# Performance work log

Measured on AMD Instinct MI355X. Metric: run time of the kernel, lower is better.

The kernel has to match this reference:

```python
import jax, jax.numpy as jnp
import numpy as np


def log_g(x):
    # log of g(x) = where(x>=0, x+0.5, sigmoid(x))
    return jnp.where(x >= 0, jnp.log(jax.nn.relu(x) + 0.5), -jax.nn.softplus(-x))


def heinsen_associative_scan_log(log_coeffs, log_values):
    a_star = jnp.cumsum(log_coeffs, axis=1)
    log_h0_plus_b_star = jax.lax.cumlogsumexp(log_values - a_star, axis=1)
    return jnp.exp(a_star + log_h0_plus_b_star)


def setup_inputs() -> dict:
    key = jax.random.key(0)
    k1, k2 = jax.random.split(key)
    B, T, D = 4, 8192, 512
    x = jax.random.normal(k1, (B, T, D), dtype=jnp.float32)
    # Linear(dim, 2*dim, bias=False); scaled like torch default init
    W = jax.random.normal(k2, (D, 2 * D), dtype=jnp.float32) * (1.0 / np.sqrt(D))
    return {"x": x, "W": W}


def reference(x, W):
    hg = jnp.einsum('btd,de->bte', x, W)  # [B,T,2D]
    hidden, gate = jnp.split(hg, 2, axis=-1)
    log_z = -jax.nn.softplus(-gate)       # log sigmoid(gate)
    log_coeffs = -jax.nn.softplus(gate)   # log (1 - sigmoid(gate))
    log_tilde_h = log_g(hidden)
    out = heinsen_associative_scan_log(log_coeffs, log_z + log_tilde_h)
    return out
```

## Files before the change

### kernel.cpp

```cpp
#include <hip/hip_runtime.h>

typedef unsigned short u16;
typedef unsigned int   u32;

typedef __bf16 bf16x8 __attribute__((ext_vector_type(8)));
typedef float  f32x4  __attribute__((ext_vector_type(4)));

#define B_DIM 4
#define T_DIM 8192
#define D_DIM 512
#define M_DIM (B_DIM * T_DIM)
#define K_DIM D_DIM
#define NC    256
#define LCH   32

__device__ __forceinline__ u16 f2bf(float f) {
  u32 u = __float_as_uint(f);
  u32 r = (u + 0x7FFFu + ((u >> 16) & 1u)) >> 16;
  return (u16)r;
}
__device__ __forceinline__ float bf2f(u16 b) {
  return __uint_as_float(((u32)b) << 16);
}

__device__ __forceinline__ void gload_lds16(const u16* g, u16* lds) {
  __builtin_amdgcn_global_load_lds(
      (const __attribute__((address_space(1))) void*)g,
      (__attribute__((address_space(3))) void*)lds, 16, 0, 0);
}


__global__ void convert_x(const float4* __restrict__ in, u16* __restrict__ out, int n4) {
  int i = blockIdx.x * blockDim.x + threadIdx.x;
  int stride = gridDim.x * blockDim.x;
  for (; i < n4; i += stride) {
    float4 f = in[i];
    u32 w0 = (u32)f2bf(f.x) | ((u32)f2bf(f.y) << 16);
    u32 w1 = (u32)f2bf(f.z) | ((u32)f2bf(f.w) << 16);
    *reinterpret_cast<uint2*>(out + (size_t)i * 4) = make_uint2(w0, w1);
  }
}

__global__ void convert_wt(const float* __restrict__ W, u16* __restrict__ wt) {
  int idx = blockIdx.x * blockDim.x + threadIdx.x;
  int n  = idx & 1023;
  int k0 = (idx >> 10) * 8;
  float f[8];
#pragma unroll
  for (int j = 0; j < 8; ++j) f[j] = W[(size_t)(k0 + j) * 1024 + n];
  u32 w[4];
#pragma unroll
  for (int j = 0; j < 4; ++j)
    w[j] = (u32)f2bf(f[2 * j]) | ((u32)f2bf(f[2 * j + 1]) << 16);
  *reinterpret_cast<uint4*>(wt + (size_t)n * 512 + k0) = make_uint4(w[0], w[1], w[2], w[3]);
}


#define BK 32
#define NT 16

__global__ __launch_bounds__(512, 4) void gemm_act(const u16* __restrict__ xb,
                                                   const u16* __restrict__ wt,
                                                   u32* __restrict__ av_buf,
                                                   float* __restrict__ Asum,
                                                   float* __restrict__ Bsum) {
  __shared__ u16 As[3][8192];
  __shared__ u16 Bs[3][4096];

  const int tid  = threadIdx.x;
  const int lane = tid & 63;
  const int wave = tid >> 6;
  const int l15  = lane & 15;
  const int lh   = lane >> 4;
  const int wr   = wave >> 1;
  const int wc   = wave & 1;
  const int m_base = blockIdx.x * 256;
  const int d0     = blockIdx.y * 64;

  const int pairl = tid >> 3;
  const int slog  = (tid & 7) ^ (pairl & 7);
  const int lrow  = (pairl << 1) | (slog >> 2);
  const int scol  = (slog & 3) << 3;
  const int garow0 = m_base + lrow;
  const int garow1 = garow0 + 128;
  const int pB = lrow >> 5;
  const int gn = ((pB & 1) ? 512 : 0) + d0 + ((pB >> 1) << 5) + (lrow & 31);
  const int ldsw = wave * 512;

  f32x4 acc[4][4];
#pragma unroll
  for (int m = 0; m < 4; ++m)
#pragma unroll
    for (int n = 0; n < 4; ++n)
      acc[m][n] = (f32x4){0.f, 0.f, 0.f, 0.f};

#define STAGE(buf, kt)                                                      \
  do {                                                                      \
    const int ko = (kt) * BK + scol;                                        \
    gload_lds16(xb + (size_t)garow0 * K_DIM + ko, &As[buf][ldsw]);          \
    gload_lds16(xb + (size_t)garow1 * K_DIM + ko, &As[buf][4096 + ldsw]);   \
    gload_lds16(wt + (size_t)gn * K_DIM + ko, &Bs[buf][ldsw]);              \
  } while (0)

#define AOFF(row) (((row) >> 1) * 64 + (((((((row) & 1) << 2) | lh)) ^ (((row) >> 1) & 7)) << 3))

#define COMPUTE(cur)                                                        \
  do {                                                                      \
    bf16x8 af[4], bfr[4];                                                   \
    _Pragma("unroll")                                                       \
    for (int m = 0; m < 4; ++m)                                             \
      af[m] = *reinterpret_cast<const bf16x8*>(&As[cur][AOFF(64 * wr + 16 * m + l15)]); \
    _Pragma("unroll")                                                       \
    for (int n = 0; n < 4; ++n)                                             \
      bfr[n] = *reinterpret_cast<const bf16x8*>(&Bs[cur][AOFF(64 * wc + 16 * n + l15)]); \
    _Pragma("unroll")                                                       \
    for (int m = 0; m < 4; ++m)                                             \
      _Pragma("unroll")                                                     \
      for (int n = 0; n < 4; ++n)                                           \
        acc[m][n] = __builtin_amdgcn_mfma_f32_16x16x32_bf16(af[m], bfr[n], acc[m][n], 0, 0, 0); \
  } while (0)

#define WAITV(N) asm volatile("s_waitcnt vmcnt(" #N ")" ::: "memory")
#define BAR()    asm volatile("s_barrier" ::: "memory")

  STAGE(0, 0);
  STAGE(1, 1);
#pragma unroll
  for (int t = 0; t < 14; ++t) {
    WAITV(3);
    BAR();
    STAGE((t + 2) % 3, t + 2);
    COMPUTE(t % 3);
  }
  WAITV(3); BAR(); COMPUTE(2);
  WAITV(0); BAR(); COMPUTE(0);
#undef STAGE
#undef COMPUTE
#undef WAITV
#undef BAR

  const int row_w = m_base + 64 * wr;
#pragma unroll
  for (int h = 0; h < 2; ++h) {
    float Ar[2][2], Br[2][2];
#pragma unroll
    for (int mm = 0; mm < 2; ++mm) {
      const int m = 2 * h + mm;
#pragma unroll
      for (int n = 0; n < 2; ++n) {
        float A = 1.f, Bv = 0.f;
        const int dch = d0 + 32 * wc + 16 * n + l15;
#pragma unroll
        for (int r = 0; r < 4; ++r) {
          float hid = acc[m][n][r];
          float gt  = acc[m][n + 2][r];
          float e   = __expf(gt);
          float inv = 1.f / (1.f + e);
          float g   = (hid >= 0.f) ? (hid + 0.5f) : (1.f / (1.f + __expf(-hid)));
          float v   = (e * inv) * g;
          u16 abf = f2bf(inv);
          u16 vbf = f2bf(v);
          const int grow = row_w + 16 * m + 4 * lh + r;
          av_buf[(size_t)grow * D_DIM + dch] = (u32)abf | ((u32)vbf << 16);
          float af = bf2f(abf), vf = bf2f(vbf);
          Bv = af * Bv + vf;
          A *= af;
        }
        Ar[n][mm] = A; Br[n][mm] = Bv;
      }
    }
#pragma unroll
    for (int n = 0; n < 2; ++n)
#pragma unroll
      for (int mm = 0; mm < 2; ++mm) {
        float A = Ar[n][mm], Bv = Br[n][mm];
#pragma unroll
        for (int d = 1; d <= 2; d <<= 1) {
          float pA = __shfl(A, lane - 16 * d);
          float pB = __shfl(Bv, lane - 16 * d);
          if (lh >= d) { Bv = A * pB + Bv; A = A * pA; }
        }
        Ar[n][mm] = A; Br[n][mm] = Bv;
      }
    if (lh == 3) {
      const int grow = row_w + 32 * h;
      const int b = grow >> 13;
      const int c = (grow & 8191) >> 5;
      const size_t o = ((size_t)(b * NC + c)) * D_DIM;
#pragma unroll
      for (int n = 0; n < 2; ++n) {
        const int dch = d0 + 32 * wc + 16 * n + l15;
        float Ac = Ar[n][0] * Ar[n][1];
        float Bc = Ar[n][1] * Br[n][0] + Br[n][1];
        Asum[o + dch] = Ac;
        Bsum[o + dch] = Bc;
      }
    }
  }
}


__global__ __launch_bounds__(256) void scan_pass2(const float* __restrict__ Asum,
                                                  const float* __restrict__ Bsum,
                                                  float* __restrict__ carry) {
  int idx = blockIdx.x * blockDim.x + threadIdx.x;
  int b = idx >> 9;
  int d = idx & 511;
  float h = 0.f;
  for (int c = 0; c < NC; ++c) {
    size_t o = ((size_t)(b * NC + c)) * D_DIM + d;
    carry[o] = h;
    h = Asum[o] * h + Bsum[o];
  }
}


__global__ __launch_bounds__(128) void scan_pass3(const u32* __restrict__ av_buf,
                                                  const float4* __restrict__ carry,
                                                  float4* __restrict__ out) {
  const int c = blockIdx.x;
  const int b = blockIdx.y;
  const int d4 = threadIdx.x;
  float4 hh = carry[((size_t)(b * NC + c)) * 128 + d4];
  float h[4] = {hh.x, hh.y, hh.z, hh.w};
  size_t base = ((size_t)b * T_DIM + (size_t)c * LCH) * D_DIM + d4 * 4;
  for (int t = 0; t < LCH; ++t) {
    uint4 w = *reinterpret_cast<const uint4*>(av_buf + base);
    h[0] = bf2f(w.x & 0xffff) * h[0] + bf2f(w.x >> 16);
    h[1] = bf2f(w.y & 0xffff) * h[1] + bf2f(w.y >> 16);
    h[2] = bf2f(w.z & 0xffff) * h[2] + bf2f(w.z >> 16);
    h[3] = bf2f(w.w & 0xffff) * h[3] + bf2f(w.w >> 16);
    out[base >> 2] = make_float4(h[0], h[1], h[2], h[3]);
    base += D_DIM;
  }
}


extern "C" void kernel_launch(void* const* d_in, const int* in_sizes, int n_in,
                              void* d_out, int out_size, void* d_ws, size_t ws_size,
                              hipStream_t stream) {
  const float* x = (const float*)d_in[0];
  const float* W = (const float*)d_in[1];
  float* out = (float*)d_out;

  char* ws = (char*)d_ws;
  u16*   xb     = (u16*)(ws + 0);
  u16*   wtp    = (u16*)(ws + 33554432);
  u32*   av_buf = (u32*)(ws + 34603008);
  float* Asum   = (float*)(ws + 101711872);
  float* Bsum   = (float*)(ws + 103809024);
  float* carry  = (float*)(ws + 105906176);
  if (ws_size < 108003328ULL) return;

  convert_x<<<2048, 256, 0, stream>>>((const float4*)x, xb, (M_DIM * K_DIM) / 4);
  convert_wt<<<256, 256, 0, stream>>>(W, wtp);
  gemm_act<<<dim3(M_DIM / 256, 8), 512, 0, stream>>>(xb, wtp, av_buf, Asum, Bsum);
  scan_pass2<<<8, 256, 0, stream>>>(Asum, Bsum, carry);
  scan_pass3<<<dim3(NC, B_DIM), 128, 0, stream>>>(av_buf, (const float4*)carry, (float4*)out);
}
```

Baseline: 114.5 us.

## Load GEMM A fragments directly from global into registers, bypassing LDS

```diff
diff --git a/kernel.cpp b/kernel.cpp
--- a/kernel.cpp
+++ b/kernel.cpp
@@ -5,6 +5,7 @@
 
 typedef __bf16 bf16x8 __attribute__((ext_vector_type(8)));
 typedef float  f32x4  __attribute__((ext_vector_type(4)));
+typedef int    i32x4  __attribute__((ext_vector_type(4)));
 
 #define B_DIM 4
 #define T_DIM 8192
@@ -64,7 +65,6 @@
                                                    u32* __restrict__ av_buf,
                                                    float* __restrict__ Asum,
                                                    float* __restrict__ Bsum) {
-  __shared__ u16 As[3][8192];
   __shared__ u16 Bs[3][4096];
 
   const int tid  = threadIdx.x;
@@ -81,12 +81,17 @@
   const int slog  = (tid & 7) ^ (pairl & 7);
   const int lrow  = (pairl << 1) | (slog >> 2);
   const int scol  = (slog & 3) << 3;
-  const int garow0 = m_base + lrow;
-  const int garow1 = garow0 + 128;
   const int pB = lrow >> 5;
   const int gn = ((pB & 1) ? 512 : 0) + d0 + ((pB >> 1) << 5) + (lrow & 31);
   const int ldsw = wave * 512;
 
+  u32 offm[4];
+#pragma unroll
+  for (int m = 0; m < 4; ++m)
+    offm[m] = (u32)(m_base + 64 * wr + 16 * m + l15) * (K_DIM * 2) + lh * 16;
+
+  i32x4 af[4];
+
   f32x4 acc[4][4];
 #pragma unroll
   for (int m = 0; m < 4; ++m)
@@ -94,50 +99,73 @@
     for (int n = 0; n < 4; ++n)
       acc[m][n] = (f32x4){0.f, 0.f, 0.f, 0.f};
 
-#define STAGE(buf, kt)                                                      \
-  do {                                                                      \
-    const int ko = (kt) * BK + scol;                                        \
-    gload_lds16(xb + (size_t)garow0 * K_DIM + ko, &As[buf][ldsw]);          \
-    gload_lds16(xb + (size_t)garow1 * K_DIM + ko, &As[buf][4096 + ldsw]);   \
-    gload_lds16(wt + (size_t)gn * K_DIM + ko, &Bs[buf][ldsw]);              \
-  } while (0)
-
-#define AOFF(row) (((row) >> 1) * 64 + (((((((row) & 1) << 2) | lh)) ^ (((row) >> 1) & 7)) << 3))
+#define STAGEB(buf, kt)                                                     \
+  gload_lds16(wt + (size_t)gn * K_DIM + (kt) * BK + scol, &Bs[buf][ldsw])
+
+#define LOADAF()                                                            \
+  do {                                                                      \
+    _Pragma("unroll")                                                       \
+    for (int m = 0; m < 4; ++m)                                             \
+      asm volatile("global_load_dwordx4 %0, %1, %2"                         \
+                   : "=v"(af[m]) : "v"(offm[m]), "s"(xb));                  \
+  } while (0)
+
+#define INCOFF()                                                            \
+  do {                                                                      \
+    _Pragma("unroll")                                                       \
+    for (int m = 0; m < 4; ++m) offm[m] += 64;                              \
+  } while (0)
+
+#define BOFF(row) (((row) >> 1) * 64 + (((((((row) & 1) << 2) | lh)) ^ (((row) >> 1) & 7)) << 3))
 
 #define COMPUTE(cur)                                                        \
   do {                                                                      \
-    bf16x8 af[4], bfr[4];                                                   \
-    _Pragma("unroll")                                                       \
-    for (int m = 0; m < 4; ++m)                                             \
-      af[m] = *reinterpret_cast<const bf16x8*>(&As[cur][AOFF(64 * wr + 16 * m + l15)]); \
+    bf16x8 bfr[4];                                                          \
     _Pragma("unroll")                                                       \
     for (int n = 0; n < 4; ++n)                                             \
-      bfr[n] = *reinterpret_cast<const bf16x8*>(&Bs[cur][AOFF(64 * wc + 16 * n + l15)]); \
-    _Pragma("unroll")                                                       \
-    for (int m = 0; m < 4; ++m)                                             \
+      bfr[n] = *reinterpret_cast<const bf16x8*>(&Bs[cur][BOFF(64 * wc + 16 * n + l15)]); \
+    _Pragma("unroll")                                                       \
+    for (int m = 0; m < 4; ++m) {                                           \
+      bf16x8 a8 = __builtin_bit_cast(bf16x8, af[m]);                        \
       _Pragma("unroll")                                                     \
       for (int n = 0; n < 4; ++n)                                           \
-        acc[m][n] = __builtin_amdgcn_mfma_f32_16x16x32_bf16(af[m], bfr[n], acc[m][n], 0, 0, 0); \
-  } while (0)
-
-#define WAITV(N) asm volatile("s_waitcnt vmcnt(" #N ")" ::: "memory")
-#define BAR()    asm volatile("s_barrier" ::: "memory")
-
-  STAGE(0, 0);
-  STAGE(1, 1);
+        acc[m][n] = __builtin_amdgcn_mfma_f32_16x16x32_bf16(a8, bfr[n], acc[m][n], 0, 0, 0); \
+    }                                                                       \
+  } while (0)
+
+#define WAITV(N)                                                            \
+  do {                                                                      \
+    asm volatile("s_waitcnt vmcnt(" #N ")" ::: "memory");                   \
+    __builtin_amdgcn_sched_barrier(0);                                      \
+  } while (0)
+#define BAR()   asm volatile("s_barrier" ::: "memory")
+#define FENCE() asm volatile("" ::: "memory")
+
+  STAGEB(0, 0);
+  FENCE();
+  LOADAF();
+  FENCE();
+  STAGEB(1, 1);
+
 #pragma unroll
   for (int t = 0; t < 14; ++t) {
-    WAITV(3);
+    WAITV(1);
     BAR();
-    STAGE((t + 2) % 3, t + 2);
     COMPUTE(t % 3);
-  }
-  WAITV(3); BAR(); COMPUTE(2);
-  WAITV(0); BAR(); COMPUTE(0);
-#undef STAGE
+    INCOFF();
+    LOADAF();
+    FENCE();
+    STAGEB((t + 2) % 3, t + 2);
+  }
+  WAITV(1); BAR(); COMPUTE(14 % 3); INCOFF(); LOADAF();
+  WAITV(0); BAR(); COMPUTE(15 % 3);
+#undef STAGEB
+#undef LOADAF
+#undef INCOFF
 #undef COMPUTE
 #undef WAITV
 #undef BAR
+#undef FENCE
 
   const int row_w = m_base + 64 * wr;
 #pragma unroll
@@ -162,9 +190,9 @@
           u16 vbf = f2bf(v);
           const int grow = row_w + 16 * m + 4 * lh + r;
           av_buf[(size_t)grow * D_DIM + dch] = (u32)abf | ((u32)vbf << 16);
-          float af = bf2f(abf), vf = bf2f(vbf);
-          Bv = af * Bv + vf;
-          A *= af;
+          float afv = bf2f(abf), vfv = bf2f(vbf);
+          Bv = afv * Bv + vfv;
+          A *= afv;
         }
         Ar[n][mm] = A; Br[n][mm] = Bv;
       }
```

Measured after the change: 142.3 us. +24.3%, slower.

## Parallelize chunk-carry scan with wave-level scan and raise MFMA priority

Applied to the files above, without the earlier changes.

```diff
diff --git a/kernel.cpp b/kernel.cpp
--- a/kernel.cpp
+++ b/kernel.cpp
@@ -113,11 +113,13 @@
     _Pragma("unroll")                                                       \
     for (int n = 0; n < 4; ++n)                                             \
       bfr[n] = *reinterpret_cast<const bf16x8*>(&Bs[cur][AOFF(64 * wc + 16 * n + l15)]); \
+    __builtin_amdgcn_s_setprio(1);                                          \
     _Pragma("unroll")                                                       \
     for (int m = 0; m < 4; ++m)                                             \
       _Pragma("unroll")                                                     \
       for (int n = 0; n < 4; ++n)                                           \
         acc[m][n] = __builtin_amdgcn_mfma_f32_16x16x32_bf16(af[m], bfr[n], acc[m][n], 0, 0, 0); \
+    __builtin_amdgcn_s_setprio(0);                                          \
   } while (0)
 
 #define WAITV(N) asm volatile("s_waitcnt vmcnt(" #N ")" ::: "memory")
@@ -162,9 +164,9 @@
           u16 vbf = f2bf(v);
           const int grow = row_w + 16 * m + 4 * lh + r;
           av_buf[(size_t)grow * D_DIM + dch] = (u32)abf | ((u32)vbf << 16);
-          float af = bf2f(abf), vf = bf2f(vbf);
-          Bv = af * Bv + vf;
-          A *= af;
+          float afv = bf2f(abf), vfv = bf2f(vbf);
+          Bv = afv * Bv + vfv;
+          A *= afv;
         }
         Ar[n][mm] = A; Br[n][mm] = Bv;
       }
@@ -203,14 +205,33 @@
 __global__ __launch_bounds__(256) void scan_pass2(const float* __restrict__ Asum,
                                                   const float* __restrict__ Bsum,
                                                   float* __restrict__ carry) {
-  int idx = blockIdx.x * blockDim.x + threadIdx.x;
-  int b = idx >> 9;
-  int d = idx & 511;
-  float h = 0.f;
-  for (int c = 0; c < NC; ++c) {
-    size_t o = ((size_t)(b * NC + c)) * D_DIM + d;
-    carry[o] = h;
-    h = Asum[o] * h + Bsum[o];
+  const int w    = (blockIdx.x << 2) + (threadIdx.x >> 6);
+  const int lane = threadIdx.x & 63;
+  const int b = w >> 9;
+  const int d = w & 511;
+  const size_t base = ((size_t)(b * NC + lane * 4)) * D_DIM + d;
+  float A[4], Bv[4];
+#pragma unroll
+  for (int i = 0; i < 4; ++i) {
+    A[i]  = Asum[base + (size_t)i * D_DIM];
+    Bv[i] = Bsum[base + (size_t)i * D_DIM];
+  }
+  float La = 1.f, Lb = 0.f;
+#pragma unroll
+  for (int i = 0; i < 4; ++i) { Lb = A[i] * Lb + Bv[i]; La *= A[i]; }
+  float Sa = La, Sb = Lb;
+#pragma unroll
+  for (int dlt = 1; dlt < 64; dlt <<= 1) {
+    float pa = __shfl_up(Sa, dlt, 64);
+    float pb = __shfl_up(Sb, dlt, 64);
+    if (lane >= dlt) { Sb = Sa * pb + Sb; Sa = Sa * pa; }
+  }
+  float Eb = __shfl_up(Sb, 1, 64);
+  float h = (lane == 0) ? 0.f : Eb;
+#pragma unroll
+  for (int i = 0; i < 4; ++i) {
+    carry[base + (size_t)i * D_DIM] = h;
+    h = A[i] * h + Bv[i];
   }
 }
 
@@ -255,6 +276,6 @@
   convert_x<<<2048, 256, 0, stream>>>((const float4*)x, xb, (M_DIM * K_DIM) / 4);
   convert_wt<<<256, 256, 0, stream>>>(W, wtp);
   gemm_act<<<dim3(M_DIM / 256, 8), 512, 0, stream>>>(xb, wtp, av_buf, Asum, Bsum);
-  scan_pass2<<<8, 256, 0, stream>>>(Asum, Bsum, carry);
+  scan_pass2<<<512, 256, 0, stream>>>(Asum, Bsum, carry);
   scan_pass3<<<dim3(NC, B_DIM), 128, 0, stream>>>(av_buf, (const float4*)carry, (float4*)out);
 }
```

Result: faster. 109.5 us (-4.3%).
